# Kernel tuning notes

Hardware: AMD Instinct MI355X
Metric: run time of the kernel (lower is better)

## Reference

```python
import jax, jax.numpy as jnp
import numpy as np

B, L, D, H, NB = 32, 200, 512, 8, 2
HD = D // H
EPS = 1e-8


def _ln(x, g, b):
    m = x.mean(-1, keepdims=True)
    v = ((x - m) ** 2).mean(-1, keepdims=True)
    return (x - m) / jnp.sqrt(v + EPS) * g + b


def setup_inputs() -> dict:
    key = jax.random.key(0)
    ks = jax.random.split(key, 12)
    w = lambda k, shape: (jax.random.normal(k, shape, jnp.float32) * 0.02)
    return {
        "x": jax.random.normal(ks[0], (B, L, D), jnp.float32),
        "timeline_mask": jnp.zeros((B, L), dtype=bool),  # True = padded
        "ln1_g": jnp.ones((NB, D), jnp.float32), "ln1_b": jnp.zeros((NB, D), jnp.float32),
        "Wq": w(ks[1], (NB, D, D)), "bq": jnp.zeros((NB, D), jnp.float32),
        "Wk": w(ks[2], (NB, D, D)), "bk": jnp.zeros((NB, D), jnp.float32),
        "Wv": w(ks[3], (NB, D, D)), "bv": jnp.zeros((NB, D), jnp.float32),
        "Wo": w(ks[4], (NB, D, D)), "bo": jnp.zeros((NB, D), jnp.float32),
        "ln2_g": jnp.ones((NB, D), jnp.float32), "ln2_b": jnp.zeros((NB, D), jnp.float32),
        "W1": w(ks[5], (NB, D, D)), "b1": jnp.zeros((NB, D), jnp.float32),
        "W2": w(ks[6], (NB, D, D)), "b2": jnp.zeros((NB, D), jnp.float32),
        "lnf_g": jnp.ones((D,), jnp.float32), "lnf_b": jnp.zeros((D,), jnp.float32),
    }


def reference(x, timeline_mask, ln1_g, ln1_b, Wq, bq, Wk, bk, Wv, bv, Wo, bo,
              ln2_g, ln2_b, W1, b1, W2, b2, lnf_g, lnf_b):
    valid = (~timeline_mask)[..., None].astype(x.dtype)  # [B,L,1]
    # causal additive bias [L,L]: 0 on/below diag, -inf above
    causal = jnp.where(jnp.tril(jnp.ones((L, L), dtype=bool)), 0.0, -jnp.inf).astype(x.dtype)
    scale = 1.0 / (HD ** 0.5)
    q = x * valid  # dropout = identity (eval)
    for i in range(NB):
        Qn = _ln(q, ln1_g[i], ln1_b[i])  # pre-attn LayerNorm (query side)
        qh = (Qn @ Wq[i] + bq[i]).reshape(B, L, H, HD)
        kh = (q @ Wk[i] + bk[i]).reshape(B, L, H, HD)
        vh = (q @ Wv[i] + bv[i]).reshape(B, L, H, HD)
        scores = jnp.einsum('bqhd,bkhd->bhqk', qh, kh) * scale + causal
        attn = jax.nn.softmax(scores, axis=-1)
        ctx = jnp.einsum('bhqk,bkhd->bqhd', attn, vh).reshape(B, L, D)
        q = ctx @ Wo[i] + bo[i] + Qn          # residual to normed Q (as in source)
        q = _ln(q, ln2_g[i], ln2_b[i])        # forward layernorm
        h = jax.nn.relu(q @ W1[i] + b1[i]) @ W2[i] + b2[i]  # 1x1 convs == per-token MLP
        q = (q + h) * valid                   # PWFF residual, then timeline mask
    return _ln(q, lnf_g, lnf_b)
```

## Files before the change

kernel.cpp:

```cpp
#include <hip/hip_runtime.h>

typedef unsigned short u16;
typedef __bf16 bfloat;
typedef bfloat bf16x8 __attribute__((ext_vector_type(8)));
typedef float f32x4 __attribute__((ext_vector_type(4)));
typedef u16 v8u16 __attribute__((ext_vector_type(8)));
typedef u16 v4u16 __attribute__((ext_vector_type(4)));

#define B_ 32
#define L_ 200
#define D_ 512
#define H_ 8
#define HD_ 64
#define M_ (B_*L_)

__device__ __forceinline__ float bf2f(u16 u) {
  union { float f; unsigned int i; } v; v.i = ((unsigned int)u) << 16; return v.f;
}
__device__ __forceinline__ u16 f2bf(float f) {
  union { float f; unsigned int i; } v; v.f = f;
  unsigned int i = v.i;
  return (u16)((i + 0x7FFFu + ((i >> 16) & 1u)) >> 16);
}
__device__ __forceinline__ bf16x8 as_bf(v8u16 v) { return __builtin_bit_cast(bf16x8, v); }

__device__ __forceinline__ void gload16(const void* g, void* l) {
  __builtin_amdgcn_global_load_lds(
      (const __attribute__((address_space(1))) void*)g,
      (__attribute__((address_space(3))) void*)l,
      16, 0, 0);
}

struct TPtrs { const float* s[12]; };

__global__ __launch_bounds__(256) void prep_kernel(
    const float* __restrict__ x, const unsigned char* __restrict__ mask,
    u16* __restrict__ qb, TPtrs tp, u16* __restrict__ dst)
{
  __shared__ float T[64][65];
  int bid = blockIdx.x;
  int t = threadIdx.x;
  if (bid < 1600) {
    size_t i = (size_t)bid * 256 + t;
    size_t base = i * 8;
    int tok = (int)(base >> 9);
    float valid = mask[tok] ? 0.f : 1.f;
    float4 v0 = *(const float4*)(x + base);
    float4 v1 = *(const float4*)(x + base + 4);
    v8u16 ob;
    ob[0]=f2bf(v0.x*valid); ob[1]=f2bf(v0.y*valid); ob[2]=f2bf(v0.z*valid); ob[3]=f2bf(v0.w*valid);
    ob[4]=f2bf(v1.x*valid); ob[5]=f2bf(v1.y*valid); ob[6]=f2bf(v1.z*valid); ob[7]=f2bf(v1.w*valid);
    *(v8u16*)(qb + base) = ob;
  } else {
    int wb   = bid - 1600;
    int mat  = wb >> 6;
    int tile = wb & 63;
    int tr = tile >> 3, tc = tile & 7;
    const float* src = tp.s[mat];
    #pragma unroll
    for (int i = 0; i < 4; i++) {
      int idx = t + i * 256;
      int row = idx >> 4, c4 = idx & 15;
      float4 v = *(const float4*)(src + (size_t)(tr * 64 + row) * 512 + tc * 64 + c4 * 4);
      T[row][c4 * 4 + 0] = v.x; T[row][c4 * 4 + 1] = v.y;
      T[row][c4 * 4 + 2] = v.z; T[row][c4 * 4 + 3] = v.w;
    }
    __syncthreads();
    u16* d = dst + (size_t)mat * 262144;
    #pragma unroll
    for (int i = 0; i < 2; i++) {
      int idx = t + i * 256;
      int row = idx >> 3, c8 = idx & 7;
      v8u16 v;
      #pragma unroll
      for (int j = 0; j < 8; j++) v[j] = f2bf(T[c8 * 8 + j][row]);
      *(v8u16*)(d + (size_t)(tc * 64 + row) * 512 + tr * 64 + c8 * 8) = v;
    }
  }
}

template<bool OUTF32>
__global__ __launch_bounds__(256) void ln_kernel(
    const u16* __restrict__ in, const float* __restrict__ g, const float* __restrict__ b,
    u16* __restrict__ outb, float* __restrict__ outf)
{
  int row  = blockIdx.x * 4 + (threadIdx.x >> 6);
  int lane = threadIdx.x & 63;
  size_t base = (size_t)row * 512 + lane * 8;
  v8u16 xv = *(const v8u16*)(in + base);
  float xs[8];
  #pragma unroll
  for (int j = 0; j < 8; j++) xs[j] = bf2f(xv[j]);
  float s = 0.f, q = 0.f;
  #pragma unroll
  for (int j = 0; j < 8; j++) { s += xs[j]; q += xs[j] * xs[j]; }
  #pragma unroll
  for (int off = 1; off < 64; off <<= 1) { s += __shfl_xor(s, off); q += __shfl_xor(q, off); }
  float mean = s * (1.f / 512.f);
  float var  = fmaxf(q * (1.f / 512.f) - mean * mean, 0.f);
  float rstd = rsqrtf(var + 1e-8f);
  float4 g0 = *(const float4*)(g + lane * 8);
  float4 g1 = *(const float4*)(g + lane * 8 + 4);
  float4 b0 = *(const float4*)(b + lane * 8);
  float4 b1 = *(const float4*)(b + lane * 8 + 4);
  float gv[8] = {g0.x,g0.y,g0.z,g0.w,g1.x,g1.y,g1.z,g1.w};
  float bv[8] = {b0.x,b0.y,b0.z,b0.w,b1.x,b1.y,b1.z,b1.w};
  if (OUTF32) {
    float of[8];
    #pragma unroll
    for (int j = 0; j < 8; j++) of[j] = (xs[j] - mean) * rstd * gv[j] + bv[j];
    *(float4*)(outf + base)     = make_float4(of[0], of[1], of[2], of[3]);
    *(float4*)(outf + base + 4) = make_float4(of[4], of[5], of[6], of[7]);
  } else {
    v8u16 ob;
    #pragma unroll
    for (int j = 0; j < 8; j++) ob[j] = f2bf((xs[j] - mean) * rstd * gv[j] + bv[j]);
    *(v8u16*)(outb + base) = ob;
  }
}

__device__ __forceinline__ void gemm_core64(
    const u16* __restrict__ A, const u16* __restrict__ Wt,
    int m0, int n0, u16* As, u16* Bs, f32x4 (&acc)[2][2])
{
  int tid = threadIdx.x, wid = tid >> 6, lane = tid & 63;
  int wr = wid >> 1, wc = wid & 1;
  int l15 = lane & 15, hi = lane >> 4;
  int sr8 = lane >> 3;
  int gsw = (lane & 7) ^ sr8;

  for (int s = 0; s < 8; s++) {
    int kk = s * 64;
    #pragma unroll
    for (int i = 0; i < 2; i++) {
      int rb = i * 32 + wid * 8;
      gload16(A  + (size_t)(m0 + rb + sr8) * 512 + kk + gsw * 8, (char*)As + rb * 128);
      gload16(Wt + (size_t)(n0 + rb + sr8) * 512 + kk + gsw * 8, (char*)Bs + rb * 128);
    }
    __syncthreads();
    #pragma unroll
    for (int ksub = 0; ksub < 2; ksub++) {
      int ga = ksub * 4 + hi;
      bf16x8 af[2], bfr[2];
      #pragma unroll
      for (int mi = 0; mi < 2; mi++) {
        int ra = wr * 32 + mi * 16 + l15;
        af[mi] = *(const bf16x8*)(As + ra * 64 + ((ga ^ (ra & 7)) * 8));
      }
      #pragma unroll
      for (int ni = 0; ni < 2; ni++) {
        int rn = wc * 32 + ni * 16 + l15;
        bfr[ni] = *(const bf16x8*)(Bs + rn * 64 + ((ga ^ (rn & 7)) * 8));
      }
      #pragma unroll
      for (int mi = 0; mi < 2; mi++)
        #pragma unroll
        for (int ni = 0; ni < 2; ni++)
          acc[mi][ni] = __builtin_amdgcn_mfma_f32_16x16x32_bf16(af[mi], bfr[ni], acc[mi][ni], 0, 0, 0);
    }
    __syncthreads();
  }
}

__device__ __forceinline__ void swz800(int bid, int& m0, int& n0) {
  int tile = (bid & 7) * 100 + (bid >> 3);
  m0 = (tile >> 3) * 64;
  n0 = (tile & 7) * 64;
}

template<bool RELU, bool HAS_RES, bool MASK>
__global__ __launch_bounds__(256) void gemm_one(
    const u16* __restrict__ A, const u16* __restrict__ Wt, const float* __restrict__ bias,
    const u16* __restrict__ res, const unsigned char* __restrict__ mask,
    u16* __restrict__ outb)
{
  __shared__ u16 As[64 * 64];
  __shared__ u16 Bs[64 * 64];
  int m0, n0;
  swz800(blockIdx.x, m0, n0);
  f32x4 acc[2][2] = {};
  gemm_core64(A, Wt, m0, n0, As, Bs, acc);

  int tid = threadIdx.x, wid = tid >> 6, lane = tid & 63;
  int wr = wid >> 1, wc = wid & 1;
  int l15 = lane & 15, hi = lane >> 4;
  #pragma unroll
  for (int ni = 0; ni < 2; ni++) {
    int gc = n0 + wc * 32 + ni * 16 + l15;
    float bvv = bias[gc];
    #pragma unroll
    for (int mi = 0; mi < 2; mi++) {
      int grb = m0 + wr * 32 + mi * 16 + hi * 4;
      #pragma unroll
      for (int r = 0; r < 4; r++) {
        int gr = grb + r;
        float v = acc[mi][ni][r] + bvv;
        if (HAS_RES) v += bf2f(res[(size_t)gr * 512 + gc]);
        if (RELU) v = fmaxf(v, 0.f);
        if (MASK) v = mask[gr] ? 0.f : v;
        outb[(size_t)gr * 512 + gc] = f2bf(v);
      }
    }
  }
}

__global__ __launch_bounds__(256) void gemm_qkv(
    const u16* __restrict__ Aq, const u16* __restrict__ Akv,
    const u16* __restrict__ Wtq, const u16* __restrict__ Wtk, const u16* __restrict__ Wtv,
    const float* __restrict__ bq, const float* __restrict__ bk, const float* __restrict__ bv,
    u16* __restrict__ outq, u16* __restrict__ outk, u16* __restrict__ outvt)
{
  __shared__ u16 As[64 * 64];
  __shared__ u16 Bs[64 * 64];
  int bid = blockIdx.x;
  int mat = bid / 800;
  int rr = bid - mat * 800;
  int m0, n0;
  swz800(rr, m0, n0);
  const u16*   A    = (mat == 0) ? Aq  : Akv;
  const u16*   Wt   = (mat == 0) ? Wtq : ((mat == 1) ? Wtk : Wtv);
  const float* bias = (mat == 0) ? bq  : ((mat == 1) ? bk  : bv);
  f32x4 acc[2][2] = {};
  gemm_core64(A, Wt, m0, n0, As, Bs, acc);

  int tid = threadIdx.x, wid = tid >> 6, lane = tid & 63;
  int wr = wid >> 1, wc = wid & 1;
  int l15 = lane & 15, hi = lane >> 4;
  if (mat == 2) {
    #pragma unroll
    for (int ni = 0; ni < 2; ni++) {
      int gc = n0 + wc * 32 + ni * 16 + l15;
      float bvv = bias[gc];
      int h = gc >> 6, hd = gc & 63;
      #pragma unroll
      for (int mi = 0; mi < 2; mi++) {
        int grb = m0 + wr * 32 + mi * 16 + hi * 4;
        #pragma unroll
        for (int r = 0; r < 4; r++) {
          int gr = grb + r;
          int b = gr / 200, l = gr - b * 200;
          outvt[((size_t)(b * 8 + h) * 64 + hd) * 224 + l] = f2bf(acc[mi][ni][r] + bvv);
        }
      }
    }
  } else {
    u16* outb = (mat == 0) ? outq : outk;
    #pragma unroll
    for (int ni = 0; ni < 2; ni++) {
      int gc = n0 + wc * 32 + ni * 16 + l15;
      float bvv = bias[gc];
      #pragma unroll
      for (int mi = 0; mi < 2; mi++) {
        int grb = m0 + wr * 32 + mi * 16 + hi * 4;
        #pragma unroll
        for (int r = 0; r < 4; r++) {
          int gr = grb + r;
          outb[(size_t)gr * 512 + gc] = f2bf(acc[mi][ni][r] + bvv);
        }
      }
    }
  }
}

__global__ __launch_bounds__(64) void attn_kernel(
    const u16* __restrict__ Qh, const u16* __restrict__ Kh,
    const u16* __restrict__ Vt, u16* __restrict__ ctx)
{
  __shared__ u16 Pb[2][16 * 32];
  int bid = blockIdx.x;
  int xcd = bid & 7, j = bid >> 3;
  int bh_hi = j / 7, s = j - bh_hi * 7;
  int bh = bh_hi * 8 + xcd;
  int b = bh >> 3, h = bh & 7;
  int lane = threadIdx.x;
  int l15 = lane & 15, hi = lane >> 4;

  const u16* Kg = Kh + (size_t)(b * L_) * D_ + h * HD_;
  const u16* Vg = Vt + (size_t)bh * 64 * 224;

  int tA = (s < 6) ? (12 - s) : 6;
  int tB = (s < 6) ? s : -1;

  for (int jj = 0; jj < 2; jj++) {
    int t = jj ? tB : tA;
    if (t < 0) break;
    int q0 = t * 16;
    int qrow = q0 + l15; if (qrow > L_ - 1) qrow = L_ - 1;
    const u16* Qg = Qh + (size_t)(b * L_ + qrow) * D_ + h * HD_ + hi * 8;
    bf16x8 aq0 = as_bf(*(const v8u16*)(Qg));
    bf16x8 aq1 = as_bf(*(const v8u16*)(Qg + 32));

    f32x4 sv[13];
    float m0[4];
    #pragma unroll
    for (int r = 0; r < 4; r++) m0[r] = -3.0e38f;

    #pragma unroll
    for (int kt = 0; kt < 13; kt++) {
      if (kt <= t) {
        const u16* kp = Kg + (size_t)(kt * 16 + l15) * D_ + hi * 8;
        bf16x8 bk0 = as_bf(*(const v8u16*)(kp));
        bf16x8 bk1 = as_bf(*(const v8u16*)(kp + 32));
        f32x4 a = {0.f, 0.f, 0.f, 0.f};
        a = __builtin_amdgcn_mfma_f32_16x16x32_bf16(aq0, bk0, a, 0, 0, 0);
        a = __builtin_amdgcn_mfma_f32_16x16x32_bf16(aq1, bk1, a, 0, 0, 0);
        #pragma unroll
        for (int r = 0; r < 4; r++) {
          int qr = q0 + hi * 4 + r;
          int kc = kt * 16 + l15;
          float val = (kc <= qr && qr < L_) ? a[r] * 0.125f : -3.0e38f;
          sv[kt][r] = val;
          m0[r] = fmaxf(m0[r], val);
        }
      }
    }
    #pragma unroll
    for (int r = 0; r < 4; r++) {
      #pragma unroll
      for (int off = 1; off < 16; off <<= 1)
        m0[r] = fmaxf(m0[r], __shfl_xor(m0[r], off));
      if (m0[r] < -1e37f) m0[r] = 0.f;
    }
    float sum[4] = {0.f, 0.f, 0.f, 0.f};
    #pragma unroll
    for (int kt = 0; kt < 13; kt++) {
      if (kt <= t) {
        #pragma unroll
        for (int r = 0; r < 4; r++) {
          float p = __expf(sv[kt][r] - m0[r]);
          sv[kt][r] = p;
          sum[r] += p;
        }
      }
    }
    #pragma unroll
    for (int r = 0; r < 4; r++) {
      #pragma unroll
      for (int off = 1; off < 16; off <<= 1) sum[r] += __shfl_xor(sum[r], off);
    }
    float inv[4];
    #pragma unroll
    for (int r = 0; r < 4; r++) inv[r] = sum[r] > 0.f ? 1.f / sum[r] : 0.f;

    int ksmax = (t + 2) >> 1;
    f32x4 acc[4] = {};
    #pragma unroll
    for (int ks = 0; ks < 7; ks++) {
      if (ks < ksmax) {
        u16* Ps = (u16*)Pb[ks & 1];
        #pragma unroll
        for (int half = 0; half < 2; half++) {
          int kt = ks * 2 + half;
          #pragma unroll
          for (int r = 0; r < 4; r++) {
            float pv = (kt <= t) ? sv[kt][r] : 0.f;
            Ps[(hi * 4 + r) * 32 + half * 16 + l15] = f2bf(pv);
          }
        }
        bf16x8 ap = as_bf(*(const v8u16*)(Ps + l15 * 32 + hi * 8));
        #pragma unroll
        for (int nt = 0; nt < 4; nt++) {
          bf16x8 bv = as_bf(*(const v8u16*)(Vg + (nt * 16 + l15) * 224 + ks * 32 + hi * 8));
          acc[nt] = __builtin_amdgcn_mfma_f32_16x16x32_bf16(ap, bv, acc[nt], 0, 0, 0);
        }
      }
    }
    #pragma unroll
    for (int nt = 0; nt < 4; nt++) {
      #pragma unroll
      for (int r = 0; r < 4; r++) {
        int qr = q0 + hi * 4 + r;
        if (qr < L_) ctx[(size_t)(b * L_ + qr) * D_ + h * HD_ + nt * 16 + l15] = f2bf(acc[nt][r] * inv[r]);
      }
    }
  }
}

extern "C" void kernel_launch(void* const* d_in, const int* in_sizes, int n_in,
                              void* d_out, int out_size, void* d_ws, size_t ws_size,
                              hipStream_t stream)
{
  (void)in_sizes; (void)n_in; (void)out_size; (void)ws_size;
  const float* x    = (const float*)d_in[0];
  const unsigned char* mask = (const unsigned char*)d_in[1];
  const float* ln1g = (const float*)d_in[2];
  const float* ln1b = (const float*)d_in[3];
  const float* Wq   = (const float*)d_in[4];
  const float* bq   = (const float*)d_in[5];
  const float* Wk   = (const float*)d_in[6];
  const float* bk   = (const float*)d_in[7];
  const float* Wv   = (const float*)d_in[8];
  const float* bv   = (const float*)d_in[9];
  const float* Wo   = (const float*)d_in[10];
  const float* bo   = (const float*)d_in[11];
  const float* ln2g = (const float*)d_in[12];
  const float* ln2b = (const float*)d_in[13];
  const float* W1   = (const float*)d_in[14];
  const float* b1   = (const float*)d_in[15];
  const float* W2   = (const float*)d_in[16];
  const float* b2   = (const float*)d_in[17];
  const float* lnfg = (const float*)d_in[18];
  const float* lnfb = (const float*)d_in[19];

  char* ws = (char*)d_ws;
  u16* Wt  = (u16*)(ws);
  u16* qb  = (u16*)(ws +  6291456);
  u16* Qn  = (u16*)(ws + 12845056);
  u16* qh  = (u16*)(ws + 19398656);
  u16* kh  = (u16*)(ws + 25952256);
  u16* vh  = (u16*)(ws + 32505856);
  u16* Vtb = (u16*)(ws + 39059456);

  TPtrs tp;
  tp.s[0] = Wq; tp.s[1] = Wq + 262144;
  tp.s[2] = Wk; tp.s[3] = Wk + 262144;
  tp.s[4] = Wv; tp.s[5] = Wv + 262144;
  tp.s[6] = Wo; tp.s[7] = Wo + 262144;
  tp.s[8] = W1; tp.s[9] = W1 + 262144;
  tp.s[10] = W2; tp.s[11] = W2 + 262144;

  prep_kernel<<<dim3(2368), dim3(256), 0, stream>>>(x, mask, qb, tp, Wt);

  for (int i = 0; i < 2; i++) {
    const u16* Wtq = Wt + (size_t)(0 + i) * 262144;
    const u16* Wtk = Wt + (size_t)(2 + i) * 262144;
    const u16* Wtv = Wt + (size_t)(4 + i) * 262144;
    const u16* Wto = Wt + (size_t)(6 + i) * 262144;
    const u16* Wt1 = Wt + (size_t)(8 + i) * 262144;
    const u16* Wt2 = Wt + (size_t)(10 + i) * 262144;

    ln_kernel<false><<<dim3(1600), dim3(256), 0, stream>>>(qb, ln1g + i * 512, ln1b + i * 512, Qn, nullptr);
    gemm_qkv<<<dim3(2400), dim3(256), 0, stream>>>(Qn, qb, Wtq, Wtk, Wtv,
                                                   bq + i * 512, bk + i * 512, bv + i * 512,
                                                   qh, kh, Vtb);
    attn_kernel<<<dim3(1792), dim3(64), 0, stream>>>(qh, kh, Vtb, vh);
    gemm_one<false,true,false><<<dim3(800), dim3(256), 0, stream>>>(vh, Wto, bo + i * 512, Qn, nullptr, qb);
    ln_kernel<false><<<dim3(1600), dim3(256), 0, stream>>>(qb, ln2g + i * 512, ln2b + i * 512, Qn, nullptr);
    gemm_one<true,false,false><<<dim3(800), dim3(256), 0, stream>>>(Qn, Wt1, b1 + i * 512, nullptr, nullptr, qh);
    gemm_one<false,true,true><<<dim3(800), dim3(256), 0, stream>>>(qh, Wt2, b2 + i * 512, Qn, mask, qb);
  }
  ln_kernel<true><<<dim3(1600), dim3(256), 0, stream>>>(qb, lnfg, lnfb, nullptr, (float*)d_out);
}
```

Before: 190.8 us.

## Fuse first LayerNorm into prep, share A tile for K/V, widen GEMM k-step

Three changes. The first block's LN1 is computed inside prep_kernel from the masked bf16 input, which removes one launch and one read of the activations. The QKV GEMM now has the K and V projections share one staged A tile, so the grid drops from 2400 to 1600 blocks and the A tile is loaded once for both. All GEMMs stage K in 128-wide steps, halving the number of barrier/load rounds at the cost of doubled LDS (up to 48KB in the QKV kernel), which can lower occupancy.

```diff
diff --git a/kernel.cpp b/kernel.cpp
--- a/kernel.cpp
+++ b/kernel.cpp
@@ -35,7 +35,8 @@
 
 __global__ __launch_bounds__(256) void prep_kernel(
     const float* __restrict__ x, const unsigned char* __restrict__ mask,
-    u16* __restrict__ qb, TPtrs tp, u16* __restrict__ dst)
+    u16* __restrict__ qb, TPtrs tp, u16* __restrict__ dst,
+    const float* __restrict__ ln1g, const float* __restrict__ ln1b, u16* __restrict__ Qn)
 {
   __shared__ float T[64][65];
   int bid = blockIdx.x;
@@ -51,6 +52,28 @@
     ob[0]=f2bf(v0.x*valid); ob[1]=f2bf(v0.y*valid); ob[2]=f2bf(v0.z*valid); ob[3]=f2bf(v0.w*valid);
     ob[4]=f2bf(v1.x*valid); ob[5]=f2bf(v1.y*valid); ob[6]=f2bf(v1.z*valid); ob[7]=f2bf(v1.w*valid);
     *(v8u16*)(qb + base) = ob;
+    int lane = t & 63;
+    float xs[8];
+    #pragma unroll
+    for (int j = 0; j < 8; j++) xs[j] = bf2f(ob[j]);
+    float s = 0.f, q = 0.f;
+    #pragma unroll
+    for (int j = 0; j < 8; j++) { s += xs[j]; q += xs[j] * xs[j]; }
+    #pragma unroll
+    for (int off = 1; off < 64; off <<= 1) { s += __shfl_xor(s, off); q += __shfl_xor(q, off); }
+    float mean = s * (1.f / 512.f);
+    float var  = fmaxf(q * (1.f / 512.f) - mean * mean, 0.f);
+    float rstd = rsqrtf(var + 1e-8f);
+    float4 g0 = *(const float4*)(ln1g + lane * 8);
+    float4 g1 = *(const float4*)(ln1g + lane * 8 + 4);
+    float4 b0 = *(const float4*)(ln1b + lane * 8);
+    float4 b1 = *(const float4*)(ln1b + lane * 8 + 4);
+    float gv[8] = {g0.x,g0.y,g0.z,g0.w,g1.x,g1.y,g1.z,g1.w};
+    float bv[8] = {b0.x,b0.y,b0.z,b0.w,b1.x,b1.y,b1.z,b1.w};
+    v8u16 qn;
+    #pragma unroll
+    for (int j = 0; j < 8; j++) qn[j] = f2bf((xs[j] - mean) * rstd * gv[j] + bv[j]);
+    *(v8u16*)(Qn + base) = qn;
   } else {
     int wb   = bid - 1600;
     int mat  = wb >> 6;
@@ -119,38 +142,46 @@
   }
 }
 
-__device__ __forceinline__ void gemm_core64(
+__device__ __forceinline__ void stage128(const u16* __restrict__ src, int r0, int kk,
+                                         u16* dstLds, int wid, int lane) {
+  int g = lane & 15;
+  #pragma unroll
+  for (int j = 0; j < 4; j++) {
+    int row = j * 16 + wid * 4 + (lane >> 4);
+    int gsrc = (g & 8) | ((g & 7) ^ (row & 7));
+    gload16(src + (size_t)(r0 + row) * 512 + kk + gsrc * 8,
+            (char*)dstLds + (j * 16 + wid * 4) * 256);
+  }
+}
+
+__device__ __forceinline__ void gemm_core128(
     const u16* __restrict__ A, const u16* __restrict__ Wt,
     int m0, int n0, u16* As, u16* Bs, f32x4 (&acc)[2][2])
 {
   int tid = threadIdx.x, wid = tid >> 6, lane = tid & 63;
   int wr = wid >> 1, wc = wid & 1;
   int l15 = lane & 15, hi = lane >> 4;
-  int sr8 = lane >> 3;
-  int gsw = (lane & 7) ^ sr8;
-
-  for (int s = 0; s < 8; s++) {
-    int kk = s * 64;
-    #pragma unroll
-    for (int i = 0; i < 2; i++) {
-      int rb = i * 32 + wid * 8;
-      gload16(A  + (size_t)(m0 + rb + sr8) * 512 + kk + gsw * 8, (char*)As + rb * 128);
-      gload16(Wt + (size_t)(n0 + rb + sr8) * 512 + kk + gsw * 8, (char*)Bs + rb * 128);
-    }
+
+  for (int s = 0; s < 4; s++) {
+    int kk = s * 128;
+    stage128(A,  m0, kk, As, wid, lane);
+    stage128(Wt, n0, kk, Bs, wid, lane);
     __syncthreads();
     #pragma unroll
-    for (int ksub = 0; ksub < 2; ksub++) {
-      int ga = ksub * 4 + hi;
+    for (int ksub = 0; ksub < 4; ksub++) {
+      int G = ksub * 4 + hi;
       bf16x8 af[2], bfr[2];
       #pragma unroll
       for (int mi = 0; mi < 2; mi++) {
         int ra = wr * 32 + mi * 16 + l15;
-        af[mi] = *(const bf16x8*)(As + ra * 64 + ((ga ^ (ra & 7)) * 8));
+        int lg = (G & 8) | ((G & 7) ^ (ra & 7));
+        af[mi] = *(const bf16x8*)(As + ra * 128 + lg * 8);
       }
       #pragma unroll
       for (int ni = 0; ni < 2; ni++) {
         int rn = wc * 32 + ni * 16 + l15;
-        bfr[ni] = *(const bf16x8*)(Bs + rn * 64 + ((ga ^ (rn & 7)) * 8));
+        int lg = (G & 8) | ((G & 7) ^ (rn & 7));
+        bfr[ni] = *(const bf16x8*)(Bs + rn * 128 + lg * 8);
       }
       #pragma unroll
       for (int mi = 0; mi < 2; mi++)
@@ -174,12 +205,12 @@
     const u16* __restrict__ res, const unsigned char* __restrict__ mask,
     u16* __restrict__ outb)
 {
-  __shared__ u16 As[64 * 64];
-  __shared__ u16 Bs[64 * 64];
+  __shared__ u16 As[64 * 128];
+  __shared__ u16 Bs[64 * 128];
   int m0, n0;
   swz800(blockIdx.x, m0, n0);
   f32x4 acc[2][2] = {};
-  gemm_core64(A, Wt, m0, n0, As, Bs, acc);
+  gemm_core128(A, Wt, m0, n0, As, Bs, acc);
 
   int tid = threadIdx.x, wid = tid >> 6, lane = tid & 63;
   int wr = wid >> 1, wc = wid & 1;
@@ -210,52 +241,83 @@
     const float* __restrict__ bq, const float* __restrict__ bk, const float* __restrict__ bv,
     u16* __restrict__ outq, u16* __restrict__ outk, u16* __restrict__ outvt)
 {
-  __shared__ u16 As[64 * 64];
-  __shared__ u16 Bs[64 * 64];
+  __shared__ u16 sh[3 * 64 * 128];
   int bid = blockIdx.x;
-  int mat = bid / 800;
-  int rr = bid - mat * 800;
-  int m0, n0;
-  swz800(rr, m0, n0);
-  const u16*   A    = (mat == 0) ? Aq  : Akv;
-  const u16*   Wt   = (mat == 0) ? Wtq : ((mat == 1) ? Wtk : Wtv);
-  const float* bias = (mat == 0) ? bq  : ((mat == 1) ? bk  : bv);
-  f32x4 acc[2][2] = {};
-  gemm_core64(A, Wt, m0, n0, As, Bs, acc);
-
+  int tile = (bid & 7) * 200 + (bid >> 3);
   int tid = threadIdx.x, wid = tid >> 6, lane = tid & 63;
   int wr = wid >> 1, wc = wid & 1;
   int l15 = lane & 15, hi = lane >> 4;
-  if (mat == 2) {
+  u16* As = sh;
+  u16* B0 = sh + 8192;
+  u16* B1 = sh + 16384;
+
+  if (tile < 800) {
+    int m0 = (tile >> 3) * 64, n0 = (tile & 7) * 64;
+    f32x4 acc[2][2] = {};
+    gemm_core128(Aq, Wtq, m0, n0, As, B0, acc);
     #pragma unroll
     for (int ni = 0; ni < 2; ni++) {
       int gc = n0 + wc * 32 + ni * 16 + l15;
-      float bvv = bias[gc];
-      int h = gc >> 6, hd = gc & 63;
+      float bvv = bq[gc];
       #pragma unroll
       for (int mi = 0; mi < 2; mi++) {
         int grb = m0 + wr * 32 + mi * 16 + hi * 4;
         #pragma unroll
+        for (int r = 0; r < 4; r++)
+          outq[(size_t)(grb + r) * 512 + gc] = f2bf(acc[mi][ni][r] + bvv);
+      }
+    }
+  } else {
+    int t2 = tile - 800;
+    int m0 = (t2 >> 3) * 64, n0 = (t2 & 7) * 64;
+    f32x4 ak[2][2] = {}, av[2][2] = {};
+    for (int s = 0; s < 4; s++) {
+      int kk = s * 128;
+      stage128(Akv, m0, kk, As, wid, lane);
+      stage128(Wtk, n0, kk, B0, wid, lane);
+      stage128(Wtv, n0, kk, B1, wid, lane);
+      __syncthreads();
+      #pragma unroll
+      for (int ksub = 0; ksub < 4; ksub++) {
+        int G = ksub * 4 + hi;
+        bf16x8 af[2], bkf[2], bvf[2];
+        #pragma unroll
+        for (int mi = 0; mi < 2; mi++) {
+          int ra = wr * 32 + mi * 16 + l15;
+          int lg = (G & 8) | ((G & 7) ^ (ra & 7));
+          af[mi] = *(const bf16x8*)(As + ra * 128 + lg * 8);
+        }
+        #pragma unroll
+        for (int ni = 0; ni < 2; ni++) {
+          int rn = wc * 32 + ni * 16 + l15;
+          int lg = (G & 8) | ((G & 7) ^ (rn & 7));
+          bkf[ni] = *(const bf16x8*)(B0 + rn * 128 + lg * 8);
+          bvf[ni] = *(const bf16x8*)(B1 + rn * 128 + lg * 8);
+        }
+        #pragma unroll
+        for (int mi = 0; mi < 2; mi++)
+          #pragma unroll
+          for (int ni = 0; ni < 2; ni++) {
+            ak[mi][ni] = __builtin_amdgcn_mfma_f32_16x16x32_bf16(af[mi], bkf[ni], ak[mi][ni], 0, 0, 0);
+            av[mi][ni] = __builtin_amdgcn_mfma_f32_16x16x32_bf16(af[mi], bvf[ni], av[mi][ni], 0, 0, 0);
+          }
+      }
+      __syncthreads();
+    }
+    #pragma unroll
+    for (int ni = 0; ni < 2; ni++) {
+      int gc = n0 + wc * 32 + ni * 16 + l15;
+      float bkv = bk[gc], bvv = bv[gc];
+      int h = gc >> 6, hd = gc & 63;
+      #pragma unroll
+      for (int mi = 0; mi < 2; mi++) {
+        int grb = m0 + wr * 32 + mi * 16 + hi * 4;
+        #pragma unroll
         for (int r = 0; r < 4; r++) {
           int gr = grb + r;
+          outk[(size_t)gr * 512 + gc] = f2bf(ak[mi][ni][r] + bkv);
           int b = gr / 200, l = gr - b * 200;
-          outvt[((size_t)(b * 8 + h) * 64 + hd) * 224 + l] = f2bf(acc[mi][ni][r] + bvv);
-        }
-      }
-    }
-  } else {
-    u16* outb = (mat == 0) ? outq : outk;
-    #pragma unroll
-    for (int ni = 0; ni < 2; ni++) {
-      int gc = n0 + wc * 32 + ni * 16 + l15;
-      float bvv = bias[gc];
-      #pragma unroll
-      for (int mi = 0; mi < 2; mi++) {
-        int grb = m0 + wr * 32 + mi * 16 + hi * 4;
-        #pragma unroll
-        for (int r = 0; r < 4; r++) {
-          int gr = grb + r;
-          outb[(size_t)gr * 512 + gc] = f2bf(acc[mi][ni][r] + bvv);
+          outvt[((size_t)(b * 8 + h) * 64 + hd) * 224 + l] = f2bf(av[mi][ni][r] + bvv);
         }
       }
     }
@@ -419,7 +481,7 @@
   tp.s[8] = W1; tp.s[9] = W1 + 262144;
   tp.s[10] = W2; tp.s[11] = W2 + 262144;
 
-  prep_kernel<<<dim3(2368), dim3(256), 0, stream>>>(x, mask, qb, tp, Wt);
+  prep_kernel<<<dim3(2368), dim3(256), 0, stream>>>(x, mask, qb, tp, Wt, ln1g, ln1b, Qn);
 
   for (int i = 0; i < 2; i++) {
     const u16* Wtq = Wt + (size_t)(0 + i) * 262144;
@@ -429,8 +491,8 @@
     const u16* Wt1 = Wt + (size_t)(8 + i) * 262144;
     const u16* Wt2 = Wt + (size_t)(10 + i) * 262144;
 
-    ln_kernel<false><<<dim3(1600), dim3(256), 0, stream>>>(qb, ln1g + i * 512, ln1b + i * 512, Qn, nullptr);
-    gemm_qkv<<<dim3(2400), dim3(256), 0, stream>>>(Qn, qb, Wtq, Wtk, Wtv,
+    if (i) ln_kernel<false><<<dim3(1600), dim3(256), 0, stream>>>(qb, ln1g + i * 512, ln1b + i * 512, Qn, nullptr);
+    gemm_qkv<<<dim3(1600), dim3(256), 0, stream>>>(Qn, qb, Wtq, Wtk, Wtv,
                                                    bq + i * 512, bk + i * 512, bv + i * 512,
                                                    qh, kh, Vtb);
     attn_kernel<<<dim3(1792), dim3(64), 0, stream>>>(qh, kh, Vtb, vh);
```

After: 177.3 us. 7.1% less time.
